# Optimization experiments

Measured on AMD Instinct MI355X. Metric: run time of the kernel, lower is better.

The kernel has to match this reference:

```python
import jax, jax.numpy as jnp
import numpy as np

N = 50000
E = 800000
F_IN = 128
HID = 128
H_HID = 4
H_OUT = 6
N_CLS = 40
NEG_SLOPE = 0.2
BN_EPS = 1e-5


def gat_conv(x, src, dst, W, a_src, a_dst, bias, concat):
    # x: [N, F_in]; W: [F_in, H*C]; a_src/a_dst: [H, C]
    H, C = a_src.shape
    h = (x @ W).reshape(N, H, C)                      # [N,H,C]
    alpha_s = jnp.sum(h * a_src[None], axis=-1)       # [N,H]
    alpha_d = jnp.sum(h * a_dst[None], axis=-1)       # [N,H]
    e = jax.nn.leaky_relu(alpha_s[src] + alpha_d[dst], NEG_SLOPE)  # [E',H]
    # segment softmax over incoming edges of each dst node
    emax = jax.ops.segment_max(e, dst, num_segments=N)
    e = jnp.exp(e - emax[dst])
    denom = jax.ops.segment_sum(e, dst, num_segments=N)
    alpha = e / (denom[dst] + 1e-16)                  # [E',H]
    out = jax.ops.segment_sum(alpha[:, :, None] * h[src], dst, num_segments=N)  # [N,H,C]
    out = out.reshape(N, H * C) if concat else out.mean(axis=1)
    return out + bias


def bn_eval(x, gamma, beta, mean, var):
    return (x - mean) * (gamma / jnp.sqrt(var + BN_EPS)) + beta


def setup_inputs() -> dict:
    key = jax.random.key(0)
    ks = jax.random.split(key, 24)
    d_h = HID * H_HID  # 512
    inp = {
        'x': jax.random.normal(ks[0], (N, F_IN), jnp.float32),
        'edge_index': jax.random.randint(ks[1], (2, E), 0, N, jnp.int64),
        # layer 0: GATConv(128 -> 128, heads=4, concat)
        'W0': jax.random.normal(ks[2], (F_IN, d_h), jnp.float32) * 0.1,
        'as0': jax.random.normal(ks[3], (H_HID, HID), jnp.float32) * 0.1,
        'ad0': jax.random.normal(ks[4], (H_HID, HID), jnp.float32) * 0.1,
        'b0': jnp.zeros((d_h,), jnp.float32),
        'g0': jax.random.uniform(ks[5], (d_h,), jnp.float32, 0.5, 1.5),
        'bt0': jax.random.normal(ks[6], (d_h,), jnp.float32) * 0.1,
        'm0': jax.random.normal(ks[7], (d_h,), jnp.float32) * 0.1,
        'v0': jax.random.uniform(ks[8], (d_h,), jnp.float32, 0.5, 1.5),
        # layer 1: GATConv(512 -> 128, heads=4, concat)
        'W1': jax.random.normal(ks[9], (d_h, d_h), jnp.float32) * 0.05,
        'as1': jax.random.normal(ks[10], (H_HID, HID), jnp.float32) * 0.1,
        'ad1': jax.random.normal(ks[11], (H_HID, HID), jnp.float32) * 0.1,
        'b1': jnp.zeros((d_h,), jnp.float32),
        'g1': jax.random.uniform(ks[12], (d_h,), jnp.float32, 0.5, 1.5),
        'bt1': jax.random.normal(ks[13], (d_h,), jnp.float32) * 0.1,
        'm1': jax.random.normal(ks[14], (d_h,), jnp.float32) * 0.1,
        'v1': jax.random.uniform(ks[15], (d_h,), jnp.float32, 0.5, 1.5),
        # layer 2: GATConv(512 -> 40, heads=6, concat=False)
        'W2': jax.random.normal(ks[16], (d_h, H_OUT * N_CLS), jnp.float32) * 0.05,
        'as2': jax.random.normal(ks[17], (H_OUT, N_CLS), jnp.float32) * 0.1,
        'ad2': jax.random.normal(ks[18], (H_OUT, N_CLS), jnp.float32) * 0.1,
        'b2': jnp.zeros((N_CLS,), jnp.float32),
    }
    return inp


def reference(x, edge_index, W0, as0, ad0, b0, g0, bt0, m0, v0,
              W1, as1, ad1, b1, g1, bt1, m1, v1,
              W2, as2, ad2, b2):
    # add self loops (PyG GATConv default add_self_loops=True)
    loop = jnp.arange(N, dtype=edge_index.dtype)
    src = jnp.concatenate([edge_index[0], loop])
    dst = jnp.concatenate([edge_index[1], loop])
    # dropout is a no-op in eval mode
    h = gat_conv(x, src, dst, W0, as0, ad0, b0, concat=True)
    h = jax.nn.elu(bn_eval(h, g0, bt0, m0, v0))
    h = gat_conv(h, src, dst, W1, as1, ad1, b1, concat=True)
    h = jax.nn.elu(bn_eval(h, g1, bt1, m1, v1))
    h = gat_conv(h, src, dst, W2, as2, ad2, b2, concat=False)
    return jax.nn.log_softmax(h, axis=-1)
```

## Files before the change

### kernel.cpp

```cpp
#include <hip/hip_runtime.h>
#include <cstdint>
#include <cstddef>

#define NN 50000
#define EE 800000
#define EPQ (EE + NN)
#define NEG_SLOPE 0.2f
#define BN_EPS 1e-5f
#define SCB 256
#define NBLK ((NN + SCB - 1) / SCB)

typedef _Float16 f16x8 __attribute__((ext_vector_type(8)));
typedef _Float16 f16x4 __attribute__((ext_vector_type(4)));
typedef _Float16 f16x2 __attribute__((ext_vector_type(2)));
typedef float f32x4 __attribute__((ext_vector_type(4)));
typedef float f32x2 __attribute__((ext_vector_type(2)));
typedef unsigned int u32;
typedef unsigned char u8;

static __device__ __forceinline__ float lrelu(float x) { return x > 0.f ? x : x * NEG_SLOPE; }

static __device__ __forceinline__ u8 f32_to_fp8(float v) {
    return (u8)(__builtin_amdgcn_cvt_pk_fp8_f32(v, v, 0, false) & 0xff);
}
static __device__ __forceinline__ void fp8x4_to_f32(u32 v, float* o) {
    f32x2 lo = __builtin_amdgcn_cvt_pk_f32_fp8(v, false);
    f32x2 hi = __builtin_amdgcn_cvt_pk_f32_fp8(v, true);
    o[0] = lo[0]; o[1] = lo[1]; o[2] = hi[0]; o[3] = hi[1];
}

static __device__ __forceinline__ void gld_lds16(const void* g, void* l) {
    __builtin_amdgcn_global_load_lds((const __attribute__((address_space(1))) u32*)g,
                                     (__attribute__((address_space(3))) u32*)l, 16, 0, 0);
}

__global__ void init_count(int* __restrict__ count) {
    int i = blockIdx.x * blockDim.x + threadIdx.x;
    if (i < NN) count[i] = 1;
}

__global__ void hist_kernel(const int* __restrict__ dst, int* __restrict__ count) {
    int e = blockIdx.x * blockDim.x + threadIdx.x;
    if (e < EE) atomicAdd(&count[dst[e]], 1);
}

__global__ __launch_bounds__(SCB) void scan1(const int* __restrict__ count,
                                             int* __restrict__ excl, int* __restrict__ bsum) {
    __shared__ int tmp[SCB];
    int b = blockIdx.x, t = threadIdx.x;
    int i = b * SCB + t;
    int v = (i < NN) ? count[i] : 0;
    tmp[t] = v;
    __syncthreads();
    for (int off = 1; off < SCB; off <<= 1) {
        int u = (t >= off) ? tmp[t - off] : 0;
        __syncthreads();
        tmp[t] += u;
        __syncthreads();
    }
    if (i < NN) excl[i] = tmp[t] - v;
    if (t == SCB - 1) bsum[b] = tmp[t];
}

__global__ __launch_bounds__(256) void scan2(const int* __restrict__ bsum, int* __restrict__ boff) {
    __shared__ int tmp[256];
    int t = threadIdx.x;
    int v = (t < NBLK) ? bsum[t] : 0;
    tmp[t] = v;
    __syncthreads();
    for (int off = 1; off < 256; off <<= 1) {
        int u = (t >= off) ? tmp[t - off] : 0;
        __syncthreads();
        tmp[t] += u;
        __syncthreads();
    }
    boff[t] = tmp[t] - v;
}

__global__ void scan3(const int* __restrict__ excl, const int* __restrict__ boff,
                      int* __restrict__ rowptr, int* __restrict__ cursor) {
    int i = blockIdx.x * blockDim.x + threadIdx.x;
    if (i < NN) {
        int r = excl[i] + boff[i / SCB];
        rowptr[i] = r;
        cursor[i] = r;
    }
    if (i == NN) rowptr[NN] = EPQ;
}

__global__ void scatter_kernel(const int* __restrict__ src, const int* __restrict__ dst,
                               int* __restrict__ cursor, int* __restrict__ csrs) {
    int e = blockIdx.x * blockDim.x + threadIdx.x;
    if (e < EE) {
        int d = dst[e];
        int slot = atomicAdd(&cursor[d], 1);
        csrs[slot] = src[e];
    } else if (e < EPQ) {
        int i = e - EE;
        int slot = atomicAdd(&cursor[i], 1);
        csrs[slot] = i;
    }
}

__global__ void cast_x_kernel(const float* __restrict__ in, _Float16* __restrict__ out, int n4) {
    int i = blockIdx.x * blockDim.x + threadIdx.x;
    if (i >= n4) return;
    f32x4 v = *(const f32x4*)(in + (size_t)i * 4);
    f16x4 o;
    o[0] = (_Float16)v[0]; o[1] = (_Float16)v[1]; o[2] = (_Float16)v[2]; o[3] = (_Float16)v[3];
    *(f16x4*)(out + (size_t)i * 4) = o;
}

__global__ __launch_bounds__(256) void tcast_kernel(const float* __restrict__ W,
                                                    _Float16* __restrict__ Wt, int K, int Nc) {
    __shared__ float tile[32][33];
    int bx = blockIdx.x * 32;
    int by = blockIdx.y * 32;
    int tx = threadIdx.x & 31, ty = threadIdx.x >> 5;
#pragma unroll
    for (int r = 0; r < 32; r += 8) {
        int k = by + ty + r, n = bx + tx;
        tile[ty + r][tx] = (k < K && n < Nc) ? W[(size_t)k * Nc + n] : 0.f;
    }
    __syncthreads();
#pragma unroll
    for (int r = 0; r < 32; r += 8) {
        int n = bx + ty + r, k = by + tx;
        if (n < Nc && k < K) Wt[(size_t)n * K + k] = (_Float16)tile[tx][ty + r];
    }
}

__global__ void prep_bn(const float* g0, const float* bt0, const float* m0, const float* v0,
                        const float* b0, const float* g1, const float* bt1, const float* m1,
                        const float* v1, const float* b1, float* sc01, float* sh01) {
    int t = threadIdx.x;
    const float *g, *bt, *m, *v, *b;
    int c;
    if (t < 512) { g = g0; bt = bt0; m = m0; v = v0; b = b0; c = t; }
    else         { g = g1; bt = bt1; m = m1; v = v1; b = b1; c = t - 512; }
    float s = g[c] * rsqrtf(v[c] + BN_EPS);
    sc01[t] = s;
    sh01[t] = (b[c] - m[c]) * s + bt[c];
}

__global__ __launch_bounds__(512) void prep_va(const _Float16* __restrict__ W0t,
                                               const _Float16* __restrict__ W1t,
                                               const _Float16* __restrict__ W2t,
                                               const float* __restrict__ as0,
                                               const float* __restrict__ ad0,
                                               const float* __restrict__ as1,
                                               const float* __restrict__ ad1,
                                               const float* __restrict__ as2,
                                               const float* __restrict__ ad2,
                                               float* __restrict__ va0, float* __restrict__ va1,
                                               float* __restrict__ va2) {
    int bid = blockIdx.x, t = threadIdx.x;
    if (bid < 8) {
        if (t >= 128) return;
        int j = bid, h = j & 3;
        const float* a = (j < 4 ? as0 : ad0) + h * 128;
        float s = 0.f;
        for (int c = 0; c < 128; c++) s += (float)W0t[(size_t)(h * 128 + c) * 128 + t] * a[c];
        va0[j * 128 + t] = s;
    } else if (bid < 16) {
        int j = bid - 8, h = j & 3;
        const float* a = (j < 4 ? as1 : ad1) + h * 128;
        float s = 0.f;
        for (int c = 0; c < 128; c++) s += (float)W1t[(size_t)(h * 128 + c) * 512 + t] * a[c];
        va1[j * 512 + t] = s;
    } else {
        int j = bid - 16, h = j % 6;
        const float* a = (j < 6 ? as2 : ad2) + h * 40;
        float s = 0.f;
        for (int c = 0; c < 40; c++) s += (float)W2t[(size_t)(h * 40 + c) * 512 + t] * a[c];
        va2[j * 512 + t] = s;
    }
}

template <bool BD, bool EPI, int OT>
__global__ __launch_bounds__(256) void gemm_t(const _Float16* __restrict__ A, int lda,
                                              const _Float16* __restrict__ Bt,
                                              void* __restrict__ Cv, int ldc, int M, int Nc,
                                              int K, const float* __restrict__ sc,
                                              const float* __restrict__ sh) {
    __shared__ __align__(16) _Float16 As[2][128 * 64];
    __shared__ __align__(16) _Float16 Bs[2][128 * 64];
    const int t = threadIdx.x;
    const int bm = blockIdx.x * 128;
    const int bn = blockIdx.y * 128;
    const int wid = t >> 6, lane = t & 63;
    const int wm = (wid >> 1) * 64, wn = (wid & 1) * 64;
    const int aoff = BD ? bn : 0;
    f32x4 acc[4][4] = {};
    const int nsteps = K >> 6;

    auto STAGE = [&](int buf, int k0) {
#pragma unroll
        for (int it = 0; it < 4; ++it) {
            int rbase = it * 32 + wid * 8;
            int row = rbase + (lane >> 3);
            int c8g = (lane & 7) ^ (row & 7);
            gld_lds16(A + (size_t)(bm + row) * lda + aoff + k0 + c8g * 8,
                      (char*)As[buf] + rbase * 128);
            gld_lds16(Bt + (size_t)(bn + row) * K + k0 + c8g * 8, (char*)Bs[buf] + rbase * 128);
        }
    };

    STAGE(0, 0);
    __syncthreads();
    int cur = 0;
    for (int s = 0; s < nsteps; ++s) {
        if (s + 1 < nsteps) STAGE(cur ^ 1, (s + 1) * 64);
#pragma unroll
        for (int ks = 0; ks < 2; ++ks) {
            f16x8 af[4], bf[4];
#pragma unroll
            for (int mi = 0; mi < 4; ++mi) {
                int row = wm + mi * 16 + (lane & 15);
                int c8 = (ks * 4 + (lane >> 4)) ^ (row & 7);
                af[mi] = *(const f16x8*)((const char*)As[cur] + row * 128 + c8 * 16);
            }
#pragma unroll
            for (int ni = 0; ni < 4; ++ni) {
                int row = wn + ni * 16 + (lane & 15);
                int c8 = (ks * 4 + (lane >> 4)) ^ (row & 7);
                bf[ni] = *(const f16x8*)((const char*)Bs[cur] + row * 128 + c8 * 16);
            }
#pragma unroll
            for (int mi = 0; mi < 4; ++mi)
#pragma unroll
                for (int ni = 0; ni < 4; ++ni)
                    acc[mi][ni] = __builtin_amdgcn_mfma_f32_16x16x32_f16(af[mi], bf[ni],
                                                                         acc[mi][ni], 0, 0, 0);
        }
        __syncthreads();
        cur ^= 1;
    }
    float scv[4], shv[4];
    if (EPI) {
#pragma unroll
        for (int ni = 0; ni < 4; ++ni) {
            int gcol = bn + wn + ni * 16 + (lane & 15);
            scv[ni] = sc[gcol];
            shv[ni] = sh[gcol];
        }
    }
#pragma unroll
    for (int mi = 0; mi < 4; ++mi) {
#pragma unroll
        for (int r = 0; r < 4; ++r) {
            int grow = bm + wm + mi * 16 + (lane >> 4) * 4 + r;
            if (grow < M) {
#pragma unroll
                for (int ni = 0; ni < 4; ++ni) {
                    int gcol = bn + wn + ni * 16 + (lane & 15);
                    if (gcol < Nc) {
                        float v = acc[mi][ni][r];
                        if (EPI) {
                            v = v * scv[ni] + shv[ni];
                            v = v > 0.f ? v : expm1f(v);
                        }
                        if constexpr (OT == 0) {
                            ((_Float16*)Cv)[(size_t)grow * ldc + gcol] = (_Float16)v;
                        } else {
                            ((u8*)Cv)[(size_t)grow * ldc + gcol] = f32_to_fp8(v);
                        }
                    }
                }
            }
        }
    }
}

__global__ __launch_bounds__(256) void alpha0(const _Float16* __restrict__ xh,
                                              const float* __restrict__ va0,
                                              float* __restrict__ asn, float* __restrict__ adn) {
    int wid = threadIdx.x >> 6, lane = threadIdx.x & 63;
    int i = blockIdx.x * 4 + wid;
    if (i >= NN) return;
    f16x2 x2 = *(const f16x2*)(xh + (size_t)i * 128 + lane * 2);
    float x0 = (float)x2[0], x1 = (float)x2[1];
    float p[8];
#pragma unroll
    for (int j = 0; j < 8; j++) {
        f32x2 v = *(const f32x2*)(va0 + j * 128 + lane * 2);
        p[j] = x0 * v[0] + x1 * v[1];
    }
#pragma unroll
    for (int off = 32; off; off >>= 1)
#pragma unroll
        for (int j = 0; j < 8; j++) p[j] += __shfl_xor(p[j], off);
    if (lane == 0) {
        f32x4 o0 = {p[0], p[1], p[2], p[3]}, o1 = {p[4], p[5], p[6], p[7]};
        *(f32x4*)(asn + (size_t)i * 4) = o0;
        *(f32x4*)(adn + (size_t)i * 4) = o1;
    }
}

template <int JH, int STR>
__global__ __launch_bounds__(256) void alpha12(const _Float16* __restrict__ feat,
                                               const float* __restrict__ va,
                                               float* __restrict__ asn, float* __restrict__ adn) {
    int wid = threadIdx.x >> 6, lane = threadIdx.x & 63;
    int i = blockIdx.x * 4 + wid;
    if (i >= NN) return;
    f16x8 x8 = *(const f16x8*)(feat + (size_t)i * 512 + lane * 8);
    float xf[8];
#pragma unroll
    for (int u = 0; u < 8; u++) xf[u] = (float)x8[u];
    float p[2 * JH];
#pragma unroll
    for (int j = 0; j < 2 * JH; j++) {
        const float* vr = va + j * 512 + lane * 8;
        f32x4 v0 = *(const f32x4*)vr;
        f32x4 v1 = *(const f32x4*)(vr + 4);
        p[j] = xf[0] * v0[0] + xf[1] * v0[1] + xf[2] * v0[2] + xf[3] * v0[3] +
               xf[4] * v1[0] + xf[5] * v1[1] + xf[6] * v1[2] + xf[7] * v1[3];
    }
#pragma unroll
    for (int off = 32; off; off >>= 1)
#pragma unroll
        for (int j = 0; j < 2 * JH; j++) p[j] += __shfl_xor(p[j], off);
    if (lane == 0) {
#pragma unroll
        for (int h = 0; h < JH; h++) {
            asn[(size_t)i * STR + h] = p[h];
            adn[(size_t)i * STR + h] = p[JH + h];
        }
    }
}

__global__ __launch_bounds__(256) void wsoft01(const float* __restrict__ asn,
                                               const float* __restrict__ adn,
                                               const int* __restrict__ rowptr,
                                               const int* __restrict__ csr,
                                               _Float16* __restrict__ wA) {
    int wid = threadIdx.x >> 6, lane = threadIdx.x & 63;
    int i = blockIdx.x * 4 + wid;
    if (i >= NN) return;
    int start = rowptr[i], end = rowptr[i + 1], deg = end - start;
    f32x4 ad = *(const f32x4*)(adn + (size_t)i * 4);
    if (deg <= 64) {
        bool v = lane < deg;
        int e = start + (v ? lane : 0);
        int s = csr[e];
        f32x4 a = *(const f32x4*)(asn + (size_t)s * 4);
        f32x4 sc;
#pragma unroll
        for (int j = 0; j < 4; j++) sc[j] = v ? lrelu(a[j] + ad[j]) : -1e30f;
        f32x4 m = sc;
#pragma unroll
        for (int off = 32; off; off >>= 1)
#pragma unroll
            for (int j = 0; j < 4; j++) m[j] = fmaxf(m[j], __shfl_xor(m[j], off));
        f32x4 wv;
#pragma unroll
        for (int j = 0; j < 4; j++) wv[j] = v ? __expf(sc[j] - m[j]) : 0.f;
        f32x4 den = wv;
#pragma unroll
        for (int off = 32; off; off >>= 1)
#pragma unroll
            for (int j = 0; j < 4; j++) den[j] += __shfl_xor(den[j], off);
        if (v) {
            f16x4 o;
#pragma unroll
            for (int j = 0; j < 4; j++) o[j] = (_Float16)(wv[j] / (den[j] + 1e-16f));
            *(f16x4*)(wA + (size_t)e * 4) = o;
        }
    } else {
        f32x4 m = {-1e30f, -1e30f, -1e30f, -1e30f};
        for (int e = start + lane; e < end; e += 64) {
            int s = csr[e];
            f32x4 a = *(const f32x4*)(asn + (size_t)s * 4);
#pragma unroll
            for (int j = 0; j < 4; j++) m[j] = fmaxf(m[j], lrelu(a[j] + ad[j]));
        }
#pragma unroll
        for (int off = 32; off; off >>= 1)
#pragma unroll
            for (int j = 0; j < 4; j++) m[j] = fmaxf(m[j], __shfl_xor(m[j], off));
        f32x4 den = {0.f, 0.f, 0.f, 0.f};
        for (int e = start + lane; e < end; e += 64) {
            int s = csr[e];
            f32x4 a = *(const f32x4*)(asn + (size_t)s * 4);
#pragma unroll
            for (int j = 0; j < 4; j++) den[j] += __expf(lrelu(a[j] + ad[j]) - m[j]);
        }
#pragma unroll
        for (int off = 32; off; off >>= 1)
#pragma unroll
            for (int j = 0; j < 4; j++) den[j] += __shfl_xor(den[j], off);
        for (int e = start + lane; e < end; e += 64) {
            int s = csr[e];
            f32x4 a = *(const f32x4*)(asn + (size_t)s * 4);
            f16x4 o;
#pragma unroll
            for (int j = 0; j < 4; j++)
                o[j] = (_Float16)(__expf(lrelu(a[j] + ad[j]) - m[j]) / (den[j] + 1e-16f));
            *(f16x4*)(wA + (size_t)e * 4) = o;
        }
    }
}

__global__ __launch_bounds__(256) void aggx(const _Float16* __restrict__ xh,
                                            const _Float16* __restrict__ wA,
                                            const int* __restrict__ rowptr,
                                            const int* __restrict__ csr,
                                            _Float16* __restrict__ xa) {
    int wid = threadIdx.x >> 6, lane = threadIdx.x & 63;
    int i = blockIdx.x * 4 + wid;
    if (i >= NN) return;
    int start = rowptr[i], end = rowptr[i + 1];
    const char* xb = (const char*)xh + lane * 4;
    float acc0[8] = {}, acc1[8] = {};
    int e = start;
    for (; e + 2 <= end; e += 2) {
        int s0 = csr[e], s1 = csr[e + 1];
        f16x4 w0 = *(const f16x4*)(wA + (size_t)e * 4);
        f16x4 w1 = *(const f16x4*)(wA + (size_t)(e + 1) * 4);
        f16x2 p0 = *(const f16x2*)(xb + (u32)s0 * 256u);
        f16x2 p1 = *(const f16x2*)(xb + (u32)s1 * 256u);
        float q00 = (float)p0[0], q01 = (float)p0[1];
        float q10 = (float)p1[0], q11 = (float)p1[1];
#pragma unroll
        for (int h = 0; h < 4; h++) {
            float wh0 = (float)w0[h], wh1 = (float)w1[h];
            acc0[h * 2] += wh0 * q00;
            acc0[h * 2 + 1] += wh0 * q01;
            acc1[h * 2] += wh1 * q10;
            acc1[h * 2 + 1] += wh1 * q11;
        }
    }
    if (e < end) {
        int s0 = csr[e];
        f16x4 w0 = *(const f16x4*)(wA + (size_t)e * 4);
        f16x2 p0 = *(const f16x2*)(xb + (u32)s0 * 256u);
        float q00 = (float)p0[0], q01 = (float)p0[1];
#pragma unroll
        for (int h = 0; h < 4; h++) {
            float wh0 = (float)w0[h];
            acc0[h * 2] += wh0 * q00;
            acc0[h * 2 + 1] += wh0 * q01;
        }
    }
#pragma unroll
    for (int h = 0; h < 4; h++) {
        f16x2 o;
        o[0] = (_Float16)(acc0[h * 2] + acc1[h * 2]);
        o[1] = (_Float16)(acc0[h * 2 + 1] + acc1[h * 2 + 1]);
        *(f16x2*)(xa + (size_t)i * 512 + h * 128 + lane * 2) = o;
    }
}

__global__ __launch_bounds__(256) void agg01(const u8* __restrict__ h,
                                             const _Float16* __restrict__ wA,
                                             const int* __restrict__ rowptr,
                                             const int* __restrict__ csr,
                                             const float* __restrict__ sc,
                                             const float* __restrict__ sh,
                                             _Float16* __restrict__ out) {
    int wid = threadIdx.x >> 6, lane = threadIdx.x & 63;
    int i = blockIdx.x * 4 + wid;
    if (i >= NN) return;
    int start = rowptr[i], end = rowptr[i + 1];
    int head = lane >> 4;
    const char* hb = (const char*)h + lane * 8;
    float acc0[8] = {}, acc1[8] = {};
    int e = start;
    for (; e + 2 <= end; e += 2) {
        int s0 = csr[e], s1 = csr[e + 1];
        float w0 = (float)wA[(size_t)e * 4 + head];
        float w1 = (float)wA[(size_t)(e + 1) * 4 + head];
        uint2 p0 = *(const uint2*)(hb + (u32)s0 * 512u);
        uint2 p1 = *(const uint2*)(hb + (u32)s1 * 512u);
        float q0[8], q1[8];
        fp8x4_to_f32(p0.x, q0); fp8x4_to_f32(p0.y, q0 + 4);
        fp8x4_to_f32(p1.x, q1); fp8x4_to_f32(p1.y, q1 + 4);
#pragma unroll
        for (int j = 0; j < 8; j++) {
            acc0[j] += w0 * q0[j];
            acc1[j] += w1 * q1[j];
        }
    }
    if (e < end) {
        int s0 = csr[e];
        float w0 = (float)wA[(size_t)e * 4 + head];
        uint2 p0 = *(const uint2*)(hb + (u32)s0 * 512u);
        float q0[8];
        fp8x4_to_f32(p0.x, q0); fp8x4_to_f32(p0.y, q0 + 4);
#pragma unroll
        for (int j = 0; j < 8; j++) acc0[j] += w0 * q0[j];
    }
    int ch = lane * 8;
    f32x4 sc0 = *(const f32x4*)(sc + ch), sc1 = *(const f32x4*)(sc + ch + 4);
    f32x4 sh0 = *(const f32x4*)(sh + ch), sh1 = *(const f32x4*)(sh + ch + 4);
    f16x8 o;
#pragma unroll
    for (int j = 0; j < 8; j++) {
        float s = (j < 4) ? sc0[j] : sc1[j - 4];
        float b = (j < 4) ? sh0[j] : sh1[j - 4];
        float val = (acc0[j] + acc1[j]) * s + b;
        val = val > 0.f ? val : expm1f(val);
        o[j] = (_Float16)val;
    }
    *(f16x8*)(out + (size_t)i * 512 + ch) = o;
}

__global__ __launch_bounds__(256) void wsoft2(const float* __restrict__ asn,
                                              const float* __restrict__ adn,
                                              const int* __restrict__ rowptr,
                                              const int* __restrict__ csr,
                                              _Float16* __restrict__ w2) {
    int wid = threadIdx.x >> 6, lane = threadIdx.x & 63;
    int i = blockIdx.x * 4 + wid;
    if (i >= NN) return;
    int start = rowptr[i], end = rowptr[i + 1], deg = end - start;
    f32x4 ad0 = *(const f32x4*)(adn + (size_t)i * 8);
    f32x4 ad1 = *(const f32x4*)(adn + (size_t)i * 8 + 4);
    float adh[6] = {ad0[0], ad0[1], ad0[2], ad0[3], ad1[0], ad1[1]};
    if (deg <= 64) {
        bool v = lane < deg;
        int e = start + (v ? lane : 0);
        int s = csr[e];
        f32x4 x0 = *(const f32x4*)(asn + (size_t)s * 8);
        f32x4 x1 = *(const f32x4*)(asn + (size_t)s * 8 + 4);
        float av[6] = {x0[0], x0[1], x0[2], x0[3], x1[0], x1[1]};
        float sc[6], m[6], wv[6], den[6];
#pragma unroll
        for (int j = 0; j < 6; j++) {
            sc[j] = v ? lrelu(av[j] + adh[j]) : -1e30f;
            m[j] = sc[j];
        }
#pragma unroll
        for (int off = 32; off; off >>= 1)
#pragma unroll
            for (int j = 0; j < 6; j++) m[j] = fmaxf(m[j], __shfl_xor(m[j], off));
#pragma unroll
        for (int j = 0; j < 6; j++) {
            wv[j] = v ? __expf(sc[j] - m[j]) : 0.f;
            den[j] = wv[j];
        }
#pragma unroll
        for (int off = 32; off; off >>= 1)
#pragma unroll
            for (int j = 0; j < 6; j++) den[j] += __shfl_xor(den[j], off);
        if (v) {
            f16x8 o;
#pragma unroll
            for (int j = 0; j < 6; j++) o[j] = (_Float16)(wv[j] / (den[j] + 1e-16f));
            o[6] = (_Float16)0.f;
            o[7] = (_Float16)0.f;
            *(f16x8*)(w2 + (size_t)e * 8) = o;
        }
    } else {
        float m[6], den[6];
#pragma unroll
        for (int j = 0; j < 6; j++) { m[j] = -1e30f; den[j] = 0.f; }
        for (int e = start + lane; e < end; e += 64) {
            int s = csr[e];
            f32x4 x0 = *(const f32x4*)(asn + (size_t)s * 8);
            f32x4 x1 = *(const f32x4*)(asn + (size_t)s * 8 + 4);
            float av[6] = {x0[0], x0[1], x0[2], x0[3], x1[0], x1[1]};
#pragma unroll
            for (int j = 0; j < 6; j++) m[j] = fmaxf(m[j], lrelu(av[j] + adh[j]));
        }
#pragma unroll
        for (int off = 32; off; off >>= 1)
#pragma unroll
            for (int j = 0; j < 6; j++) m[j] = fmaxf(m[j], __shfl_xor(m[j], off));
        for (int e = start + lane; e < end; e += 64) {
            int s = csr[e];
            f32x4 x0 = *(const f32x4*)(asn + (size_t)s * 8);
            f32x4 x1 = *(const f32x4*)(asn + (size_t)s * 8 + 4);
            float av[6] = {x0[0], x0[1], x0[2], x0[3], x1[0], x1[1]};
#pragma unroll
            for (int j = 0; j < 6; j++) den[j] += __expf(lrelu(av[j] + adh[j]) - m[j]);
        }
#pragma unroll
        for (int off = 32; off; off >>= 1)
#pragma unroll
            for (int j = 0; j < 6; j++) den[j] += __shfl_xor(den[j], off);
        for (int e = start + lane; e < end; e += 64) {
            int s = csr[e];
            f32x4 x0 = *(const f32x4*)(asn + (size_t)s * 8);
            f32x4 x1 = *(const f32x4*)(asn + (size_t)s * 8 + 4);
            float av[6] = {x0[0], x0[1], x0[2], x0[3], x1[0], x1[1]};
            f16x8 o;
#pragma unroll
            for (int j = 0; j < 6; j++)
                o[j] = (_Float16)(__expf(lrelu(av[j] + adh[j]) - m[j]) / (den[j] + 1e-16f));
            o[6] = (_Float16)0.f;
            o[7] = (_Float16)0.f;
            *(f16x8*)(w2 + (size_t)e * 8) = o;
        }
    }
}

__global__ __launch_bounds__(256) void agg2f(const u8* __restrict__ h2,
                                             const _Float16* __restrict__ w2,
                                             const int* __restrict__ rowptr,
                                             const int* __restrict__ csr,
                                             const float* __restrict__ b2,
                                             float* __restrict__ out) {
    __shared__ float sval[4][240];
    int wid = threadIdx.x >> 6, lane = threadIdx.x & 63;
    int i = blockIdx.x * 4 + wid;
    if (i < NN) {
        int start = rowptr[i], end = rowptr[i + 1];
        int head = (lane < 60) ? (lane / 10) : 0;
        const char* hb = (const char*)h2 + lane * 4;
        float a0[4] = {}, a1[4] = {};
        int e = start;
        for (; e + 2 <= end; e += 2) {
            int s0 = csr[e], s1 = csr[e + 1];
            float w0 = (float)w2[(size_t)e * 8 + head];
            float w1 = (float)w2[(size_t)(e + 1) * 8 + head];
            u32 p0 = *(const u32*)(hb + (u32)s0 * 256u);
            u32 p1 = *(const u32*)(hb + (u32)s1 * 256u);
            float q0[4], q1[4];
            fp8x4_to_f32(p0, q0);
            fp8x4_to_f32(p1, q1);
#pragma unroll
            for (int j = 0; j < 4; j++) {
                a0[j] += w0 * q0[j];
                a1[j] += w1 * q1[j];
            }
        }
        if (e < end) {
            int s0 = csr[e];
            float w0 = (float)w2[(size_t)e * 8 + head];
            u32 p0 = *(const u32*)(hb + (u32)s0 * 256u);
            float q0[4];
            fp8x4_to_f32(p0, q0);
#pragma unroll
            for (int j = 0; j < 4; j++) a0[j] += w0 * q0[j];
        }
        if (lane < 60) {
#pragma unroll
            for (int j = 0; j < 4; j++) sval[wid][lane * 4 + j] = a0[j] + a1[j];
        }
    }
    __syncthreads();
    if (i < NN) {
        float v = -INFINITY;
        if (lane < 40) {
            float s = 0.f;
#pragma unroll
            for (int hh = 0; hh < 6; hh++) s += sval[wid][hh * 40 + lane];
            v = s * (1.0f / 6.0f) + b2[lane];
        }
        float mm = v;
#pragma unroll
        for (int off = 32; off; off >>= 1) mm = fmaxf(mm, __shfl_xor(mm, off));
        float se = (lane < 40) ? __expf(v - mm) : 0.f;
#pragma unroll
        for (int off = 32; off; off >>= 1) se += __shfl_xor(se, off);
        if (lane < 40) out[(size_t)i * 40 + lane] = v - mm - logf(se);
    }
}

extern "C" void kernel_launch(void* const* d_in, const int* in_sizes, int n_in,
                              void* d_out, int out_size, void* d_ws, size_t ws_size,
                              hipStream_t stream) {
    const float* x   = (const float*)d_in[0];
    const int*   ei  = (const int*)d_in[1];
    const float* W0  = (const float*)d_in[2];
    const float* as0 = (const float*)d_in[3];
    const float* ad0 = (const float*)d_in[4];
    const float* b0  = (const float*)d_in[5];
    const float* g0  = (const float*)d_in[6];
    const float* bt0 = (const float*)d_in[7];
    const float* m0  = (const float*)d_in[8];
    const float* v0  = (const float*)d_in[9];
    const float* W1  = (const float*)d_in[10];
    const float* as1 = (const float*)d_in[11];
    const float* ad1 = (const float*)d_in[12];
    const float* b1  = (const float*)d_in[13];
    const float* g1  = (const float*)d_in[14];
    const float* bt1 = (const float*)d_in[15];
    const float* m1  = (const float*)d_in[16];
    const float* v1  = (const float*)d_in[17];
    const float* W2  = (const float*)d_in[18];
    const float* as2w = (const float*)d_in[19];
    const float* ad2w = (const float*)d_in[20];
    const float* b2  = (const float*)d_in[21];
    float* out = (float*)d_out;
    const int* srcv = ei;
    const int* dstv = ei + EE;

    char* w = (char*)d_ws;
    auto carve = [&](size_t bytes) {
        char* p = w;
        w += (bytes + 255) & ~(size_t)255;
        return p;
    };
    _Float16* xh   = (_Float16*)carve((size_t)NN * 128 * 2);
    _Float16* hA   = (_Float16*)carve((size_t)NN * 512 * 2);
    _Float16* actB = (_Float16*)carve((size_t)NN * 512 * 2);
    _Float16* W0t  = (_Float16*)carve((size_t)512 * 128 * 2);
    _Float16* W1t  = (_Float16*)carve((size_t)512 * 512 * 2);
    _Float16* W2t  = (_Float16*)carve((size_t)240 * 512 * 2);
    float* va0  = (float*)carve((size_t)8 * 128 * 4);
    float* va1  = (float*)carve((size_t)8 * 512 * 4);
    float* va2  = (float*)carve((size_t)12 * 512 * 4);
    float* sc01 = (float*)carve((size_t)1024 * 4);
    float* sh01 = (float*)carve((size_t)1024 * 4);
    float* asn  = (float*)carve((size_t)NN * 8 * 4);
    float* adn  = (float*)carve((size_t)NN * 8 * 4);
    _Float16* wE = (_Float16*)carve((size_t)EPQ * 8 * 2);
    int* count  = (int*)carve((size_t)(NN + 8) * 4);
    int* excl   = (int*)carve((size_t)(NN + 8) * 4);
    int* bsum   = (int*)carve((size_t)512 * 4);
    int* boff   = (int*)carve((size_t)512 * 4);
    int* rowptr = (int*)carve((size_t)(NN + 8) * 4);
    int* cursor = (int*)carve((size_t)(NN + 8) * 4);
    int* csrs   = (int*)carve((size_t)EPQ * 4);
    _Float16* xa = hA;
    u8* h1q  = (u8*)hA;
    u8* h2q  = (u8*)hA;

    init_count<<<(NN + 255) / 256, 256, 0, stream>>>(count);
    hist_kernel<<<(EE + 255) / 256, 256, 0, stream>>>(dstv, count);
    scan1<<<NBLK, SCB, 0, stream>>>(count, excl, bsum);
    scan2<<<1, 256, 0, stream>>>(bsum, boff);
    scan3<<<(NN + 256) / 256, 256, 0, stream>>>(excl, boff, rowptr, cursor);
    scatter_kernel<<<(EPQ + 255) / 256, 256, 0, stream>>>(srcv, dstv, cursor, csrs);

    cast_x_kernel<<<(NN * 128 / 4 + 255) / 256, 256, 0, stream>>>(x, xh, NN * 128 / 4);
    tcast_kernel<<<dim3(16, 4), 256, 0, stream>>>(W0, W0t, 128, 512);
    tcast_kernel<<<dim3(16, 16), 256, 0, stream>>>(W1, W1t, 512, 512);
    tcast_kernel<<<dim3(8, 16), 256, 0, stream>>>(W2, W2t, 512, 240);
    prep_bn<<<1, 1024, 0, stream>>>(g0, bt0, m0, v0, b0, g1, bt1, m1, v1, b1, sc01, sh01);
    prep_va<<<28, 512, 0, stream>>>(W0t, W1t, W2t, as0, ad0, as1, ad1, as2w, ad2w, va0, va1, va2);

    const int MT = (NN + 127) / 128;
    const int NG = (NN + 3) / 4;

    alpha0<<<NG, 256, 0, stream>>>(xh, va0, asn, adn);
    wsoft01<<<NG, 256, 0, stream>>>(asn, adn, rowptr, csrs, wE);
    aggx<<<NG, 256, 0, stream>>>(xh, wE, rowptr, csrs, xa);
    gemm_t<true, true, 0><<<dim3(MT, 4), 256, 0, stream>>>(xa, 512, W0t, actB, 512, NN, 512, 128,
                                                           sc01, sh01);

    gemm_t<false, false, 1><<<dim3(MT, 4), 256, 0, stream>>>(actB, 512, W1t, h1q, 512, NN, 512,
                                                             512, nullptr, nullptr);
    alpha12<4, 4><<<NG, 256, 0, stream>>>(actB, va1, asn, adn);
    wsoft01<<<NG, 256, 0, stream>>>(asn, adn, rowptr, csrs, wE);
    agg01<<<NG, 256, 0, stream>>>(h1q, wE, rowptr, csrs, sc01 + 512, sh01 + 512, actB);

    gemm_t<false, false, 1><<<dim3(MT, 2), 256, 0, stream>>>(actB, 512, W2t, h2q, 256, NN, 240,
                                                             512, nullptr, nullptr);
    alpha12<6, 8><<<NG, 256, 0, stream>>>(actB, va2, asn, adn);
    wsoft2<<<NG, 256, 0, stream>>>(asn, adn, rowptr, csrs, wE);
    agg2f<<<NG, 256, 0, stream>>>(h2q, wE, rowptr, csrs, b2, out);
}
```

Baseline: 638.5 us.

## Fuse edge softmax into aggregation kernels and gather layer-0 input in FP8

The separate edge-softmax kernels (wsoft01, wsoft2) are removed. Each aggregation kernel now computes the per-destination softmax weights itself, keeping them in LDS for nodes with degree up to 64 and recomputing them inline for higher-degree nodes. This avoids writing and re-reading a per-edge weight array and saves three kernel launches. Layer 0's aggregation also gathers an FP8 copy of x written by the cast kernel instead of the FP16 copy, halving gather bytes at some precision cost. The layer-0 loop loses its two-edge unrolling, which may reduce memory-level parallelism.

```diff
diff --git a/kernel.cpp b/kernel.cpp
--- a/kernel.cpp
+++ b/kernel.cpp
@@ -17,6 +17,7 @@
 typedef float f32x2 __attribute__((ext_vector_type(2)));
 typedef unsigned int u32;
 typedef unsigned char u8;
+typedef unsigned short u16;
 
 static __device__ __forceinline__ float lrelu(float x) { return x > 0.f ? x : x * NEG_SLOPE; }
 
@@ -102,13 +103,17 @@
     }
 }
 
-__global__ void cast_x_kernel(const float* __restrict__ in, _Float16* __restrict__ out, int n4) {
+__global__ void cast_x_kernel(const float* __restrict__ in, _Float16* __restrict__ out,
+                              u32* __restrict__ outq, int n4) {
     int i = blockIdx.x * blockDim.x + threadIdx.x;
     if (i >= n4) return;
     f32x4 v = *(const f32x4*)(in + (size_t)i * 4);
     f16x4 o;
     o[0] = (_Float16)v[0]; o[1] = (_Float16)v[1]; o[2] = (_Float16)v[2]; o[3] = (_Float16)v[3];
     *(f16x4*)(out + (size_t)i * 4) = o;
+    u32 q = __builtin_amdgcn_cvt_pk_fp8_f32(v[0], v[1], 0, false);
+    q = __builtin_amdgcn_cvt_pk_fp8_f32(v[2], v[3], q, true);
+    outq[i] = q;
 }
 
 __global__ __launch_bounds__(256) void tcast_kernel(const float* __restrict__ W,
@@ -330,147 +335,179 @@
     }
 }
 
-__global__ __launch_bounds__(256) void wsoft01(const float* __restrict__ asn,
-                                               const float* __restrict__ adn,
-                                               const int* __restrict__ rowptr,
-                                               const int* __restrict__ csr,
-                                               _Float16* __restrict__ wA) {
+__global__ __launch_bounds__(256) void aggx(const u8* __restrict__ xq,
+                                            const float* __restrict__ asn,
+                                            const float* __restrict__ adn,
+                                            const int* __restrict__ rowptr,
+                                            const int* __restrict__ csr,
+                                            _Float16* __restrict__ xa) {
+    __shared__ __align__(8) _Float16 wsl[4][64][4];
     int wid = threadIdx.x >> 6, lane = threadIdx.x & 63;
     int i = blockIdx.x * 4 + wid;
     if (i >= NN) return;
     int start = rowptr[i], end = rowptr[i + 1], deg = end - start;
+    bool fastp = deg <= 64;
     f32x4 ad = *(const f32x4*)(adn + (size_t)i * 4);
-    if (deg <= 64) {
+    f32x4 m4, rd4;
+    if (fastp) {
         bool v = lane < deg;
         int e = start + (v ? lane : 0);
         int s = csr[e];
         f32x4 a = *(const f32x4*)(asn + (size_t)s * 4);
-        f32x4 sc;
-#pragma unroll
-        for (int j = 0; j < 4; j++) sc[j] = v ? lrelu(a[j] + ad[j]) : -1e30f;
-        f32x4 m = sc;
+        f32x4 sc4, mm, wv, dn;
+#pragma unroll
+        for (int j = 0; j < 4; j++) { sc4[j] = v ? lrelu(a[j] + ad[j]) : -1e30f; mm[j] = sc4[j]; }
 #pragma unroll
         for (int off = 32; off; off >>= 1)
 #pragma unroll
-            for (int j = 0; j < 4; j++) m[j] = fmaxf(m[j], __shfl_xor(m[j], off));
-        f32x4 wv;
-#pragma unroll
-        for (int j = 0; j < 4; j++) wv[j] = v ? __expf(sc[j] - m[j]) : 0.f;
-        f32x4 den = wv;
+            for (int j = 0; j < 4; j++) mm[j] = fmaxf(mm[j], __shfl_xor(mm[j], off));
+#pragma unroll
+        for (int j = 0; j < 4; j++) { wv[j] = v ? __expf(sc4[j] - mm[j]) : 0.f; dn[j] = wv[j]; }
 #pragma unroll
         for (int off = 32; off; off >>= 1)
 #pragma unroll
-            for (int j = 0; j < 4; j++) den[j] += __shfl_xor(den[j], off);
-        if (v) {
-            f16x4 o;
-#pragma unroll
-            for (int j = 0; j < 4; j++) o[j] = (_Float16)(wv[j] / (den[j] + 1e-16f));
-            *(f16x4*)(wA + (size_t)e * 4) = o;
-        }
+            for (int j = 0; j < 4; j++) dn[j] += __shfl_xor(dn[j], off);
+        f16x4 o;
+#pragma unroll
+        for (int j = 0; j < 4; j++) o[j] = (_Float16)(wv[j] / (dn[j] + 1e-16f));
+        *(f16x4*)&wsl[wid][lane][0] = o;
     } else {
-        f32x4 m = {-1e30f, -1e30f, -1e30f, -1e30f};
+        f32x4 mm = {-1e30f, -1e30f, -1e30f, -1e30f};
         for (int e = start + lane; e < end; e += 64) {
             int s = csr[e];
             f32x4 a = *(const f32x4*)(asn + (size_t)s * 4);
 #pragma unroll
-            for (int j = 0; j < 4; j++) m[j] = fmaxf(m[j], lrelu(a[j] + ad[j]));
+            for (int j = 0; j < 4; j++) mm[j] = fmaxf(mm[j], lrelu(a[j] + ad[j]));
         }
 #pragma unroll
         for (int off = 32; off; off >>= 1)
 #pragma unroll
-            for (int j = 0; j < 4; j++) m[j] = fmaxf(m[j], __shfl_xor(m[j], off));
-        f32x4 den = {0.f, 0.f, 0.f, 0.f};
+            for (int j = 0; j < 4; j++) mm[j] = fmaxf(mm[j], __shfl_xor(mm[j], off));
+        f32x4 dn = {0.f, 0.f, 0.f, 0.f};
         for (int e = start + lane; e < end; e += 64) {
             int s = csr[e];
             f32x4 a = *(const f32x4*)(asn + (size_t)s * 4);
 #pragma unroll
-            for (int j = 0; j < 4; j++) den[j] += __expf(lrelu(a[j] + ad[j]) - m[j]);
+            for (int j = 0; j < 4; j++) dn[j] += __expf(lrelu(a[j] + ad[j]) - mm[j]);
         }
 #pragma unroll
         for (int off = 32; off; off >>= 1)
 #pragma unroll
-            for (int j = 0; j < 4; j++) den[j] += __shfl_xor(den[j], off);
-        for (int e = start + lane; e < end; e += 64) {
-            int s = csr[e];
-            f32x4 a = *(const f32x4*)(asn + (size_t)s * 4);
-            f16x4 o;
-#pragma unroll
-            for (int j = 0; j < 4; j++)
-                o[j] = (_Float16)(__expf(lrelu(a[j] + ad[j]) - m[j]) / (den[j] + 1e-16f));
-            *(f16x4*)(wA + (size_t)e * 4) = o;
-        }
-    }
-}
-
-__global__ __launch_bounds__(256) void aggx(const _Float16* __restrict__ xh,
-                                            const _Float16* __restrict__ wA,
-                                            const int* __restrict__ rowptr,
-                                            const int* __restrict__ csr,
-                                            _Float16* __restrict__ xa) {
-    int wid = threadIdx.x >> 6, lane = threadIdx.x & 63;
-    int i = blockIdx.x * 4 + wid;
-    if (i >= NN) return;
-    int start = rowptr[i], end = rowptr[i + 1];
-    const char* xb = (const char*)xh + lane * 4;
-    float acc0[8] = {}, acc1[8] = {};
-    int e = start;
-    for (; e + 2 <= end; e += 2) {
-        int s0 = csr[e], s1 = csr[e + 1];
-        f16x4 w0 = *(const f16x4*)(wA + (size_t)e * 4);
-        f16x4 w1 = *(const f16x4*)(wA + (size_t)(e + 1) * 4);
-        f16x2 p0 = *(const f16x2*)(xb + (u32)s0 * 256u);
-        f16x2 p1 = *(const f16x2*)(xb + (u32)s1 * 256u);
-        float q00 = (float)p0[0], q01 = (float)p0[1];
-        float q10 = (float)p1[0], q11 = (float)p1[1];
+            for (int j = 0; j < 4; j++) dn[j] += __shfl_xor(dn[j], off);
+        m4 = mm;
+#pragma unroll
+        for (int j = 0; j < 4; j++) rd4[j] = 1.f / (dn[j] + 1e-16f);
+    }
+    const char* xb = (const char*)xq + lane * 2;
+    float acc[8] = {};
+    for (int e = start; e < end; e++) {
+        int s = csr[e];
+        float w[4];
+        if (fastp) {
+            f16x4 wv4 = *(const f16x4*)&wsl[wid][e - start][0];
+#pragma unroll
+            for (int h = 0; h < 4; h++) w[h] = (float)wv4[h];
+        } else {
+#pragma unroll
+            for (int h = 0; h < 4; h++)
+                w[h] = __expf(lrelu(asn[(size_t)s * 4 + h] + ad[h]) - m4[h]) * rd4[h];
+        }
+        u16 pv = *(const u16*)(xb + (u32)s * 128u);
+        f32x2 q = __builtin_amdgcn_cvt_pk_f32_fp8((u32)pv, false);
 #pragma unroll
         for (int h = 0; h < 4; h++) {
-            float wh0 = (float)w0[h], wh1 = (float)w1[h];
-            acc0[h * 2] += wh0 * q00;
-            acc0[h * 2 + 1] += wh0 * q01;
-            acc1[h * 2] += wh1 * q10;
-            acc1[h * 2 + 1] += wh1 * q11;
-        }
-    }
-    if (e < end) {
-        int s0 = csr[e];
-        f16x4 w0 = *(const f16x4*)(wA + (size_t)e * 4);
-        f16x2 p0 = *(const f16x2*)(xb + (u32)s0 * 256u);
-        float q00 = (float)p0[0], q01 = (float)p0[1];
-#pragma unroll
-        for (int h = 0; h < 4; h++) {
-            float wh0 = (float)w0[h];
-            acc0[h * 2] += wh0 * q00;
-            acc0[h * 2 + 1] += wh0 * q01;
+            acc[h * 2] += w[h] * q[0];
+            acc[h * 2 + 1] += w[h] * q[1];
         }
     }
 #pragma unroll
     for (int h = 0; h < 4; h++) {
         f16x2 o;
-        o[0] = (_Float16)(acc0[h * 2] + acc1[h * 2]);
-        o[1] = (_Float16)(acc0[h * 2 + 1] + acc1[h * 2 + 1]);
+        o[0] = (_Float16)acc[h * 2];
+        o[1] = (_Float16)acc[h * 2 + 1];
         *(f16x2*)(xa + (size_t)i * 512 + h * 128 + lane * 2) = o;
     }
 }
 
 __global__ __launch_bounds__(256) void agg01(const u8* __restrict__ h,
-                                             const _Float16* __restrict__ wA,
+                                             const float* __restrict__ asn,
+                                             const float* __restrict__ adn,
                                              const int* __restrict__ rowptr,
                                              const int* __restrict__ csr,
                                              const float* __restrict__ sc,
                                              const float* __restrict__ sh,
                                              _Float16* __restrict__ out) {
+    __shared__ __align__(8) _Float16 wsl[4][64][4];
     int wid = threadIdx.x >> 6, lane = threadIdx.x & 63;
     int i = blockIdx.x * 4 + wid;
     if (i >= NN) return;
-    int start = rowptr[i], end = rowptr[i + 1];
+    int start = rowptr[i], end = rowptr[i + 1], deg = end - start;
+    bool fastp = deg <= 64;
+    f32x4 ad = *(const f32x4*)(adn + (size_t)i * 4);
+    f32x4 m4, rd4;
+    if (fastp) {
+        bool v = lane < deg;
+        int e = start + (v ? lane : 0);
+        int s = csr[e];
+        f32x4 a = *(const f32x4*)(asn + (size_t)s * 4);
+        f32x4 sc4, mm, wv, dn;
+#pragma unroll
+        for (int j = 0; j < 4; j++) { sc4[j] = v ? lrelu(a[j] + ad[j]) : -1e30f; mm[j] = sc4[j]; }
+#pragma unroll
+        for (int off = 32; off; off >>= 1)
+#pragma unroll
+            for (int j = 0; j < 4; j++) mm[j] = fmaxf(mm[j], __shfl_xor(mm[j], off));
+#pragma unroll
+        for (int j = 0; j < 4; j++) { wv[j] = v ? __expf(sc4[j] - mm[j]) : 0.f; dn[j] = wv[j]; }
+#pragma unroll
+        for (int off = 32; off; off >>= 1)
+#pragma unroll
+            for (int j = 0; j < 4; j++) dn[j] += __shfl_xor(dn[j], off);
+        f16x4 o;
+#pragma unroll
+        for (int j = 0; j < 4; j++) o[j] = (_Float16)(wv[j] / (dn[j] + 1e-16f));
+        *(f16x4*)&wsl[wid][lane][0] = o;
+    } else {
+        f32x4 mm = {-1e30f, -1e30f, -1e30f, -1e30f};
+        for (int e = start + lane; e < end; e += 64) {
+            int s = csr[e];
+            f32x4 a = *(const f32x4*)(asn + (size_t)s * 4);
+#pragma unroll
+            for (int j = 0; j < 4; j++) mm[j] = fmaxf(mm[j], lrelu(a[j] + ad[j]));
+        }
+#pragma unroll
+        for (int off = 32; off; off >>= 1)
+#pragma unroll
+            for (int j = 0; j < 4; j++) mm[j] = fmaxf(mm[j], __shfl_xor(mm[j], off));
+        f32x4 dn = {0.f, 0.f, 0.f, 0.f};
+        for (int e = start + lane; e < end; e += 64) {
+            int s = csr[e];
+            f32x4 a = *(const f32x4*)(asn + (size_t)s * 4);
+#pragma unroll
+            for (int j = 0; j < 4; j++) dn[j] += __expf(lrelu(a[j] + ad[j]) - mm[j]);
+        }
+#pragma unroll
+        for (int off = 32; off; off >>= 1)
+#pragma unroll
+            for (int j = 0; j < 4; j++) dn[j] += __shfl_xor(dn[j], off);
+        m4 = mm;
+#pragma unroll
+        for (int j = 0; j < 4; j++) rd4[j] = 1.f / (dn[j] + 1e-16f);
+    }
     int head = lane >> 4;
     const char* hb = (const char*)h + lane * 8;
     float acc0[8] = {}, acc1[8] = {};
     int e = start;
     for (; e + 2 <= end; e += 2) {
         int s0 = csr[e], s1 = csr[e + 1];
-        float w0 = (float)wA[(size_t)e * 4 + head];
-        float w1 = (float)wA[(size_t)(e + 1) * 4 + head];
+        float w0, w1;
+        if (fastp) {
+            w0 = (float)wsl[wid][e - start][head];
+            w1 = (float)wsl[wid][e + 1 - start][head];
+        } else {
+            w0 = __expf(lrelu(asn[(size_t)s0 * 4 + head] + ad[head]) - m4[head]) * rd4[head];
+            w1 = __expf(lrelu(asn[(size_t)s1 * 4 + head] + ad[head]) - m4[head]) * rd4[head];
+        }
         uint2 p0 = *(const uint2*)(hb + (u32)s0 * 512u);
         uint2 p1 = *(const uint2*)(hb + (u32)s1 * 512u);
         float q0[8], q1[8];
@@ -484,7 +521,9 @@
     }
     if (e < end) {
         int s0 = csr[e];
-        float w0 = (float)wA[(size_t)e * 4 + head];
+        float w0;
+        if (fastp) w0 = (float)wsl[wid][e - start][head];
+        else w0 = __expf(lrelu(asn[(size_t)s0 * 4 + head] + ad[head]) - m4[head]) * rd4[head];
         uint2 p0 = *(const uint2*)(hb + (u32)s0 * 512u);
         float q0[8];
         fp8x4_to_f32(p0.x, q0); fp8x4_to_f32(p0.y, q0 + 4);
@@ -506,115 +545,98 @@
     *(f16x8*)(out + (size_t)i * 512 + ch) = o;
 }
 
-__global__ __launch_bounds__(256) void wsoft2(const float* __restrict__ asn,
-                                              const float* __restrict__ adn,
-                                              const int* __restrict__ rowptr,
-                                              const int* __restrict__ csr,
-                                              _Float16* __restrict__ w2) {
+__global__ __launch_bounds__(256) void agg2f(const u8* __restrict__ h2,
+                                             const float* __restrict__ asn,
+                                             const float* __restrict__ adn,
+                                             const int* __restrict__ rowptr,
+                                             const int* __restrict__ csr,
+                                             const float* __restrict__ b2,
+                                             float* __restrict__ out) {
+    __shared__ __align__(16) _Float16 wsl[4][64][8];
+    __shared__ float sval[4][240];
     int wid = threadIdx.x >> 6, lane = threadIdx.x & 63;
     int i = blockIdx.x * 4 + wid;
-    if (i >= NN) return;
-    int start = rowptr[i], end = rowptr[i + 1], deg = end - start;
-    f32x4 ad0 = *(const f32x4*)(adn + (size_t)i * 8);
-    f32x4 ad1 = *(const f32x4*)(adn + (size_t)i * 8 + 4);
-    float adh[6] = {ad0[0], ad0[1], ad0[2], ad0[3], ad1[0], ad1[1]};
-    if (deg <= 64) {
-        bool v = lane < deg;
-        int e = start + (v ? lane : 0);
-        int s = csr[e];
-        f32x4 x0 = *(const f32x4*)(asn + (size_t)s * 8);
-        f32x4 x1 = *(const f32x4*)(asn + (size_t)s * 8 + 4);
-        float av[6] = {x0[0], x0[1], x0[2], x0[3], x1[0], x1[1]};
-        float sc[6], m[6], wv[6], den[6];
-#pragma unroll
-        for (int j = 0; j < 6; j++) {
-            sc[j] = v ? lrelu(av[j] + adh[j]) : -1e30f;
-            m[j] = sc[j];
-        }
-#pragma unroll
-        for (int off = 32; off; off >>= 1)
-#pragma unroll
-            for (int j = 0; j < 6; j++) m[j] = fmaxf(m[j], __shfl_xor(m[j], off));
-#pragma unroll
-        for (int j = 0; j < 6; j++) {
-            wv[j] = v ? __expf(sc[j] - m[j]) : 0.f;
-            den[j] = wv[j];
-        }
-#pragma unroll
-        for (int off = 32; off; off >>= 1)
-#pragma unroll
-            for (int j = 0; j < 6; j++) den[j] += __shfl_xor(den[j], off);
-        if (v) {
-            f16x8 o;
-#pragma unroll
-            for (int j = 0; j < 6; j++) o[j] = (_Float16)(wv[j] / (den[j] + 1e-16f));
-            o[6] = (_Float16)0.f;
-            o[7] = (_Float16)0.f;
-            *(f16x8*)(w2 + (size_t)e * 8) = o;
-        }
-    } else {
-        float m[6], den[6];
-#pragma unroll
-        for (int j = 0; j < 6; j++) { m[j] = -1e30f; den[j] = 0.f; }
-        for (int e = start + lane; e < end; e += 64) {
+    if (i < NN) {
+        int start = rowptr[i], end = rowptr[i + 1], deg = end - start;
+        bool fastp = deg <= 64;
+        f32x4 ad0 = *(const f32x4*)(adn + (size_t)i * 8);
+        f32x4 ad1 = *(const f32x4*)(adn + (size_t)i * 8 + 4);
+        float adh[6] = {ad0[0], ad0[1], ad0[2], ad0[3], ad1[0], ad1[1]};
+        float m6[6], rd6[6];
+        if (fastp) {
+            bool v = lane < deg;
+            int e = start + (v ? lane : 0);
             int s = csr[e];
             f32x4 x0 = *(const f32x4*)(asn + (size_t)s * 8);
             f32x4 x1 = *(const f32x4*)(asn + (size_t)s * 8 + 4);
             float av[6] = {x0[0], x0[1], x0[2], x0[3], x1[0], x1[1]};
-#pragma unroll
-            for (int j = 0; j < 6; j++) m[j] = fmaxf(m[j], lrelu(av[j] + adh[j]));
-        }
-#pragma unroll
-        for (int off = 32; off; off >>= 1)
-#pragma unroll
-            for (int j = 0; j < 6; j++) m[j] = fmaxf(m[j], __shfl_xor(m[j], off));
-        for (int e = start + lane; e < end; e += 64) {
-            int s = csr[e];
-            f32x4 x0 = *(const f32x4*)(asn + (size_t)s * 8);
-            f32x4 x1 = *(const f32x4*)(asn + (size_t)s * 8 + 4);
-            float av[6] = {x0[0], x0[1], x0[2], x0[3], x1[0], x1[1]};
-#pragma unroll
-            for (int j = 0; j < 6; j++) den[j] += __expf(lrelu(av[j] + adh[j]) - m[j]);
-        }
-#pragma unroll
-        for (int off = 32; off; off >>= 1)
-#pragma unroll
-            for (int j = 0; j < 6; j++) den[j] += __shfl_xor(den[j], off);
-        for (int e = start + lane; e < end; e += 64) {
-            int s = csr[e];
-            f32x4 x0 = *(const f32x4*)(asn + (size_t)s * 8);
-            f32x4 x1 = *(const f32x4*)(asn + (size_t)s * 8 + 4);
-            float av[6] = {x0[0], x0[1], x0[2], x0[3], x1[0], x1[1]};
+            float sc6[6], mm[6], wv[6], dn[6];
+#pragma unroll
+            for (int j = 0; j < 6; j++) {
+                sc6[j] = v ? lrelu(av[j] + adh[j]) : -1e30f;
+                mm[j] = sc6[j];
+            }
+#pragma unroll
+            for (int off = 32; off; off >>= 1)
+#pragma unroll
+                for (int j = 0; j < 6; j++) mm[j] = fmaxf(mm[j], __shfl_xor(mm[j], off));
+#pragma unroll
+            for (int j = 0; j < 6; j++) { wv[j] = v ? __expf(sc6[j] - mm[j]) : 0.f; dn[j] = wv[j]; }
+#pragma unroll
+            for (int off = 32; off; off >>= 1)
+#pragma unroll
+                for (int j = 0; j < 6; j++) dn[j] += __shfl_xor(dn[j], off);
             f16x8 o;
 #pragma unroll
-            for (int j = 0; j < 6; j++)
-                o[j] = (_Float16)(__expf(lrelu(av[j] + adh[j]) - m[j]) / (den[j] + 1e-16f));
+            for (int j = 0; j < 6; j++) o[j] = (_Float16)(wv[j] / (dn[j] + 1e-16f));
             o[6] = (_Float16)0.f;
             o[7] = (_Float16)0.f;
-            *(f16x8*)(w2 + (size_t)e * 8) = o;
-        }
-    }
-}
-
-__global__ __launch_bounds__(256) void agg2f(const u8* __restrict__ h2,
-                                             const _Float16* __restrict__ w2,
-                                             const int* __restrict__ rowptr,
-                                             const int* __restrict__ csr,
-                                             const float* __restrict__ b2,
-                                             float* __restrict__ out) {
-    __shared__ float sval[4][240];
-    int wid = threadIdx.x >> 6, lane = threadIdx.x & 63;
-    int i = blockIdx.x * 4 + wid;
-    if (i < NN) {
-        int start = rowptr[i], end = rowptr[i + 1];
+            *(f16x8*)&wsl[wid][lane][0] = o;
+        } else {
+            float mm[6], dn[6];
+#pragma unroll
+            for (int j = 0; j < 6; j++) { mm[j] = -1e30f; dn[j] = 0.f; }
+            for (int e = start + lane; e < end; e += 64) {
+                int s = csr[e];
+                f32x4 x0 = *(const f32x4*)(asn + (size_t)s * 8);
+                f32x4 x1 = *(const f32x4*)(asn + (size_t)s * 8 + 4);
+                float av[6] = {x0[0], x0[1], x0[2], x0[3], x1[0], x1[1]};
+#pragma unroll
+                for (int j = 0; j < 6; j++) mm[j] = fmaxf(mm[j], lrelu(av[j] + adh[j]));
+            }
+#pragma unroll
+            for (int off = 32; off; off >>= 1)
+#pragma unroll
+                for (int j = 0; j < 6; j++) mm[j] = fmaxf(mm[j], __shfl_xor(mm[j], off));
+            for (int e = start + lane; e < end; e += 64) {
+                int s = csr[e];
+                f32x4 x0 = *(const f32x4*)(asn + (size_t)s * 8);
+                f32x4 x1 = *(const f32x4*)(asn + (size_t)s * 8 + 4);
+                float av[6] = {x0[0], x0[1], x0[2], x0[3], x1[0], x1[1]};
+#pragma unroll
+                for (int j = 0; j < 6; j++) dn[j] += __expf(lrelu(av[j] + adh[j]) - mm[j]);
+            }
+#pragma unroll
+            for (int off = 32; off; off >>= 1)
+#pragma unroll
+                for (int j = 0; j < 6; j++) dn[j] += __shfl_xor(dn[j], off);
+#pragma unroll
+            for (int j = 0; j < 6; j++) { m6[j] = mm[j]; rd6[j] = 1.f / (dn[j] + 1e-16f); }
+        }
         int head = (lane < 60) ? (lane / 10) : 0;
         const char* hb = (const char*)h2 + lane * 4;
         float a0[4] = {}, a1[4] = {};
         int e = start;
         for (; e + 2 <= end; e += 2) {
             int s0 = csr[e], s1 = csr[e + 1];
-            float w0 = (float)w2[(size_t)e * 8 + head];
-            float w1 = (float)w2[(size_t)(e + 1) * 8 + head];
+            float w0, w1;
+            if (fastp) {
+                w0 = (float)wsl[wid][e - start][head];
+                w1 = (float)wsl[wid][e + 1 - start][head];
+            } else {
+                w0 = __expf(lrelu(asn[(size_t)s0 * 8 + head] + adh[head]) - m6[head]) * rd6[head];
+                w1 = __expf(lrelu(asn[(size_t)s1 * 8 + head] + adh[head]) - m6[head]) * rd6[head];
+            }
             u32 p0 = *(const u32*)(hb + (u32)s0 * 256u);
             u32 p1 = *(const u32*)(hb + (u32)s1 * 256u);
             float q0[4], q1[4];
@@ -628,7 +650,9 @@
         }
         if (e < end) {
             int s0 = csr[e];
-            float w0 = (float)w2[(size_t)e * 8 + head];
+            float w0;
+            if (fastp) w0 = (float)wsl[wid][e - start][head];
+            else w0 = __expf(lrelu(asn[(size_t)s0 * 8 + head] + adh[head]) - m6[head]) * rd6[head];
             u32 p0 = *(const u32*)(hb + (u32)s0 * 256u);
             float q0[4];
             fp8x4_to_f32(p0, q0);
@@ -695,6 +719,7 @@
         return p;
     };
     _Float16* xh   = (_Float16*)carve((size_t)NN * 128 * 2);
+    u32* xq        = (u32*)carve((size_t)NN * 128);
     _Float16* hA   = (_Float16*)carve((size_t)NN * 512 * 2);
     _Float16* actB = (_Float16*)carve((size_t)NN * 512 * 2);
     _Float16* W0t  = (_Float16*)carve((size_t)512 * 128 * 2);
@@ -707,7 +732,6 @@
     float* sh01 = (float*)carve((size_t)1024 * 4);
     float* asn  = (float*)carve((size_t)NN * 8 * 4);
     float* adn  = (float*)carve((size_t)NN * 8 * 4);
-    _Float16* wE = (_Float16*)carve((size_t)EPQ * 8 * 2);
     int* count  = (int*)carve((size_t)(NN + 8) * 4);
     int* excl   = (int*)carve((size_t)(NN + 8) * 4);
     int* bsum   = (int*)carve((size_t)512 * 4);
@@ -726,7 +750,7 @@
     scan3<<<(NN + 256) / 256, 256, 0, stream>>>(excl, boff, rowptr, cursor);
     scatter_kernel<<<(EPQ + 255) / 256, 256, 0, stream>>>(srcv, dstv, cursor, csrs);
 
-    cast_x_kernel<<<(NN * 128 / 4 + 255) / 256, 256, 0, stream>>>(x, xh, NN * 128 / 4);
+    cast_x_kernel<<<(NN * 128 / 4 + 255) / 256, 256, 0, stream>>>(x, xh, xq, NN * 128 / 4);
     tcast_kernel<<<dim3(16, 4), 256, 0, stream>>>(W0, W0t, 128, 512);
     tcast_kernel<<<dim3(16, 16), 256, 0, stream>>>(W1, W1t, 512, 512);
     tcast_kernel<<<dim3(8, 16), 256, 0, stream>>>(W2, W2t, 512, 240);
@@ -737,20 +761,17 @@
     const int NG = (NN + 3) / 4;
 
     alpha0<<<NG, 256, 0, stream>>>(xh, va0, asn, adn);
-    wsoft01<<<NG, 256, 0, stream>>>(asn, adn, rowptr, csrs, wE);
-    aggx<<<NG, 256, 0, stream>>>(xh, wE, rowptr, csrs, xa);
+    aggx<<<NG, 256, 0, stream>>>((const u8*)xq, asn, adn, rowptr, csrs, xa);
     gemm_t<true, true, 0><<<dim3(MT, 4), 256, 0, stream>>>(xa, 512, W0t, actB, 512, NN, 512, 128,
                                                            sc01, sh01);
 
     gemm_t<false, false, 1><<<dim3(MT, 4), 256, 0, stream>>>(actB, 512, W1t, h1q, 512, NN, 512,
                                                              512, nullptr, nullptr);
     alpha12<4, 4><<<NG, 256, 0, stream>>>(actB, va1, asn, adn);
-    wsoft01<<<NG, 256, 0, stream>>>(asn, adn, rowptr, csrs, wE);
-    agg01<<<NG, 256, 0, stream>>>(h1q, wE, rowptr, csrs, sc01 + 512, sh01 + 512, actB);
+    agg01<<<NG, 256, 0, stream>>>(h1q, asn, adn, rowptr, csrs, sc01 + 512, sh01 + 512, actB);
 
     gemm_t<false, false, 1><<<dim3(MT, 2), 256, 0, stream>>>(actB, 512, W2t, h2q, 256, NN, 240,
                                                              512, nullptr, nullptr);
     alpha12<6, 8><<<NG, 256, 0, stream>>>(actB, va2, asn, adn);
-    wsoft2<<<NG, 256, 0, stream>>>(asn, adn, rowptr, csrs, wE);
-    agg2f<<<NG, 256, 0, stream>>>(h2q, wE, rowptr, csrs, b2, out);
-}
+    agg2f<<<NG, 256, 0, stream>>>(h2q, asn, adn, rowptr, csrs, b2, out);
+}
```

New measurement: 603.1 us. 5.6% less time.
